# Kernel tuning notes

Measured on AMD Instinct MI355X. Metric: run time of the kernel, lower is better.

## Reference

```python
import jax, jax.numpy as jnp
import numpy as np
from jax import lax

B = 32768
D_IN = 512
D_DENSE = 256
T, F = 16, 16
H1, H2 = 128, 32
N_CLASSES = 10
BN_EPS = 1e-3


def _lstm_scan(xs, Wx, Wh, b):
    """Keras-style LSTM. xs: [B,T,F]; Wx: [F,4H]; Wh: [H,4H]; b: [4H].
    Gate order (Keras): i, f, g(candidate), o. Returns hs: [T,B,H]."""
    Bn = xs.shape[0]
    H = Wh.shape[0]
    # precompute input projections for all timesteps (one big GEMM)
    zx = jnp.einsum('btf,fg->tbg', xs, Wx) + b  # [T,B,4H]

    def step(carry, zx_t):
        h, c = carry
        z = zx_t + h @ Wh  # [B,4H]
        i, f, g, o = jnp.split(z, 4, axis=-1)
        i = jax.nn.sigmoid(i)
        f = jax.nn.sigmoid(f)
        g = jnp.tanh(g)
        o = jax.nn.sigmoid(o)
        c = f * c + i * g
        h = o * jnp.tanh(c)
        return (h, c), h

    h0 = jnp.zeros((Bn, H), xs.dtype)
    c0 = jnp.zeros((Bn, H), xs.dtype)
    (_, _), hs = lax.scan(step, (h0, c0), zx)
    return hs  # [T,B,H]


def setup_inputs() -> dict:
    key = jax.random.key(0)
    ks = jax.random.split(key, 12)
    s = lambda *sh: 1.0 / np.sqrt(sh[0])
    inp = {
        'x': jax.random.normal(ks[0], (B, D_IN), jnp.float32),
        'W_d1': jax.random.normal(ks[1], (D_IN, D_DENSE), jnp.float32) * s(D_IN),
        'b_d1': jnp.zeros((D_DENSE,), jnp.float32),
        'bn_gamma': jnp.ones((D_DENSE,), jnp.float32),
        'bn_beta': jnp.zeros((D_DENSE,), jnp.float32),
        'bn_mean': jax.random.normal(ks[2], (D_DENSE,), jnp.float32) * 0.1,
        'bn_var': jax.random.uniform(ks[3], (D_DENSE,), jnp.float32, 0.5, 1.5),
        'Wx1': jax.random.normal(ks[4], (F, 4 * H1), jnp.float32) * s(F),
        'Wh1': jax.random.normal(ks[5], (H1, 4 * H1), jnp.float32) * s(H1),
        'b1': jnp.zeros((4 * H1,), jnp.float32),
        'Wx2': jax.random.normal(ks[6], (H1, 4 * H2), jnp.float32) * s(H1),
        'Wh2': jax.random.normal(ks[7], (H2, 4 * H2), jnp.float32) * s(H2),
        'b2': jnp.zeros((4 * H2,), jnp.float32),
        'W_d2': jax.random.normal(ks[8], (H2, N_CLASSES), jnp.float32) * s(H2),
        'b_d2': jnp.zeros((N_CLASSES,), jnp.float32),
    }
    return inp


def reference(x, W_d1, b_d1, bn_gamma, bn_beta, bn_mean, bn_var,
              Wx1, Wh1, b1, Wx2, Wh2, b2, W_d2, b_d2):
    # Dense(256)
    h = x @ W_d1 + b_d1  # [B,256]
    # BatchNorm (inference: moving stats), eps=1e-3 (Keras default)
    h = (h - bn_mean) * (bn_gamma * lax.rsqrt(bn_var + BN_EPS)) + bn_beta
    # LeakyReLU(0.2)
    h = jnp.where(h >= 0, h, 0.2 * h)
    # Reshape to [B,16,16]
    seq = h.reshape(-1, T, F)
    # LSTM(128, return_sequences=True); dropout is inference no-op
    hs1 = _lstm_scan(seq, Wx1, Wh1, b1)            # [T,B,128]
    # LSTM(32, return_sequences=False)
    hs2 = _lstm_scan(jnp.swapaxes(hs1, 0, 1), Wx2, Wh2, b2)  # [T,B,32]
    h_last = hs2[-1]                                # [B,32]
    # Dense(10, softmax)
    logits = h_last @ W_d2 + b_d2
    return jax.nn.softmax(logits, axis=-1)
```

## Files before the change

### kernel.cpp

```cpp
#include <hip/hip_runtime.h>
#include <hip/hip_bf16.h>
#include <stdint.h>


typedef short bf16x8 __attribute__((ext_vector_type(8)));
typedef float f32x4 __attribute__((ext_vector_type(4)));
typedef unsigned short ushort_t;

#define NTHR 512

__device__ __forceinline__ ushort_t f2bf(float f) {
    unsigned u = __float_as_uint(f);
    u = u + 0x7fffu + ((u >> 16) & 1u);
    return (ushort_t)(u >> 16);
}
__device__ __forceinline__ float bf2f(ushort_t h) {
    return __uint_as_float(((unsigned)h) << 16);
}
__device__ __forceinline__ ushort_t planev(float v, int plane) {
    ushort_t hi = f2bf(v);
    if (plane == 0) return hi;
    return f2bf(v - bf2f(hi));
}
__device__ __forceinline__ int foff(int nt, int KC, int kc, int plane, int lane) {
    return (((nt * KC + kc) * 2 + plane) * 64 + lane) * 8;
}
__device__ __forceinline__ f32x4 mfma16(bf16x8 a, bf16x8 b, f32x4 c) {
    return __builtin_amdgcn_mfma_f32_16x16x32_bf16(a, b, c, 0, 0, 0);
}
__device__ __forceinline__ float sigm(float x) { return 1.0f / (1.0f + __expf(-x)); }
__device__ __forceinline__ float tanhc(float x) {
    x = fminf(15.0f, fmaxf(-15.0f, x));
    float e = __expf(2.0f * x);
    return (e - 1.0f) / (e + 1.0f);
}

__global__ void prep_weights(const float* __restrict__ Wd1, const float* __restrict__ Wx1,
                             const float* __restrict__ Wh1, const float* __restrict__ Wx2,
                             const float* __restrict__ Wh2, const float* __restrict__ Wd2,
                             ushort_t* __restrict__ wd1f, ushort_t* __restrict__ wh1f,
                             ushort_t* __restrict__ wx1f, ushort_t* __restrict__ w2f,
                             ushort_t* __restrict__ wd2f) {
    const int i = blockIdx.x * blockDim.x + threadIdx.x;
    const int j = i & 7;
    const int lane = (i >> 3) & 63;
    const int plane = (i >> 9) & 1;
    const int rest = i >> 10;
    const int krow = ((lane >> 4) << 3) + j;
    const int ncol = lane & 15;
    {
        const int kc = rest & 15, nt = rest >> 4;
        const int k = kc * 32 + krow, n = nt * 16 + ncol;
        wd1f[i] = planev(Wd1[k * 256 + n], plane);
    }
    if (i < 131072) {
        const int kc = rest & 3, nt = rest >> 2;
        const int k = kc * 32 + krow, n = nt * 16 + ncol;
        wh1f[i] = planev(Wh1[k * 512 + n], plane);
    }
    if (i < 32768) {
        const int nt = rest;
        const int k = krow, n = nt * 16 + ncol;
        const float v = (k < 16) ? Wx1[k * 512 + n] : 0.f;
        wx1f[i] = planev(v, plane);
    }
    if (i < 40960) {
        const int kc = rest % 5, nt = rest / 5;
        const int k = kc * 32 + krow, n = nt * 16 + ncol;
        const float v = (k < 32) ? Wh2[k * 128 + n] : Wx2[(k - 32) * 128 + n];
        w2f[i] = planev(v, plane);
    }
    if (i < 1024) {
        const int k = krow, n = ncol;
        const float v = (n < 10) ? Wd2[k * 10 + n] : 0.f;
        wd2f[i] = planev(v, plane);
    }
}

__global__ __launch_bounds__(NTHR, 2) void dense1_kernel(
    const float* __restrict__ X, const float* __restrict__ bd1,
    const float* __restrict__ gam, const float* __restrict__ bet,
    const float* __restrict__ mu, const float* __restrict__ var,
    const ushort_t* __restrict__ wd1f, ushort_t* __restrict__ sfrag) {
    __shared__ __align__(16) ushort_t Xs[2][64][40];
    const int tid = threadIdx.x;
    const int lane = tid & 63, w = tid >> 6;
    const int l4 = lane >> 4, l15 = lane & 15;
    const int blk = blockIdx.x;
    const long rowbase = (long)blk * 64;

    float bias[2];
#pragma unroll
    for (int ct = 0; ct < 2; ++ct) bias[ct] = bd1[w * 32 + ct * 16 + l15];
    f32x4 acc[4][2];
#pragma unroll
    for (int rt = 0; rt < 4; ++rt)
#pragma unroll
        for (int ct = 0; ct < 2; ++ct) { f32x4 a = {bias[ct], bias[ct], bias[ct], bias[ct]}; acc[rt][ct] = a; }

    const int srow = tid >> 3;
    const int sc4 = tid & 7;

#pragma unroll 1
    for (int kc = 0; kc < 16; ++kc) {
        if (kc) __syncthreads();
        const float4 xv = *reinterpret_cast<const float4*>(X + (rowbase + srow) * 512 + kc * 32 + sc4 * 4);
        float x4[4] = {xv.x, xv.y, xv.z, xv.w};
        ushort_t hs[4], ls[4];
#pragma unroll
        for (int q = 0; q < 4; ++q) { hs[q] = f2bf(x4[q]); ls[q] = f2bf(x4[q] - bf2f(hs[q])); }
        *reinterpret_cast<ushort4*>(&Xs[0][srow][sc4 * 4]) = make_ushort4(hs[0], hs[1], hs[2], hs[3]);
        *reinterpret_cast<ushort4*>(&Xs[1][srow][sc4 * 4]) = make_ushort4(ls[0], ls[1], ls[2], ls[3]);
        __syncthreads();

        bf16x8 Ah[4], Al[4];
#pragma unroll
        for (int rt = 0; rt < 4; ++rt) {
            Ah[rt] = *reinterpret_cast<const bf16x8*>(&Xs[0][rt * 16 + l15][l4 * 8]);
            Al[rt] = *reinterpret_cast<const bf16x8*>(&Xs[1][rt * 16 + l15][l4 * 8]);
        }
#pragma unroll
        for (int ct = 0; ct < 2; ++ct) {
            const int nt = w * 2 + ct;
            bf16x8 Bh = *reinterpret_cast<const bf16x8*>(wd1f + foff(nt, 16, kc, 0, lane));
            bf16x8 Bl = *reinterpret_cast<const bf16x8*>(wd1f + foff(nt, 16, kc, 1, lane));
#pragma unroll
            for (int rt = 0; rt < 4; ++rt) {
                acc[rt][ct] = mfma16(Ah[rt], Bh, acc[rt][ct]);
                acc[rt][ct] = mfma16(Ah[rt], Bl, acc[rt][ct]);
                acc[rt][ct] = mfma16(Al[rt], Bh, acc[rt][ct]);
            }
        }
    }

#pragma unroll
    for (int ct = 0; ct < 2; ++ct) {
        const int col = w * 32 + ct * 16 + l15;
        const float sc = gam[col] * rsqrtf(var[col] + 1e-3f);
        const float sh = bet[col] - mu[col] * sc;
        const int t = col >> 4, f = col & 15;
        const int jp = f & 7;
#pragma unroll
        for (int rt = 0; rt < 4; ++rt) {
            const long rtg = (long)blk * 4 + rt;
#pragma unroll
            for (int jd = 0; jd < 4; ++jd) {
                float v = acc[rt][ct][jd] * sc + sh;
                v = (v >= 0.f) ? v : 0.2f * v;
                const int rowin = l4 * 4 + jd;
                const int lanep = rowin + ((f >> 3) << 4);
                const long base = (((rtg * 16 + t) * 2 + 0) * 32 + lanep) * 8 + jp;
                const ushort_t hi = f2bf(v);
                sfrag[base] = hi;
                sfrag[base + 256] = f2bf(v - bf2f(hi));
            }
        }
    }
}

__global__ __launch_bounds__(NTHR, 1) void lstm_kernel(
    const ushort_t* __restrict__ wh1f, const ushort_t* __restrict__ wx1f,
    const ushort_t* __restrict__ w2f, const ushort_t* __restrict__ wd2f,
    const ushort_t* __restrict__ sfrag, const float* __restrict__ b1,
    const float* __restrict__ b2, const float* __restrict__ bd2,
    float* __restrict__ out) {
    __shared__ __align__(16) ushort_t A[2][64][168];
    __shared__ float C1[64][132];
    const int tid = threadIdx.x;
    const int lane = tid & 63, w = tid >> 6;
    const int l4 = lane >> 4, l15 = lane & 15;
    const int blk = blockIdx.x;

    {
        unsigned long long* p = (unsigned long long*)&A[0][0][0];
#pragma unroll 4
        for (int i = tid; i < 2 * 64 * 168 / 4; i += NTHR) p[i] = 0ull;
        float* q = &C1[0][0];
#pragma unroll 4
        for (int i = tid; i < 64 * 132; i += NTHR) q[i] = 0.f;
    }

    float c2[4];
#pragma unroll
    for (int q = 0; q < 4; ++q) c2[q] = 0.f;

    const int u1 = w * 16 + l15;
    float b1g[4];
#pragma unroll
    for (int g = 0; g < 4; ++g) b1g[g] = b1[g * 128 + u1];
    const int rt2 = w & 3;
    const int u2base = (w >> 2) * 16;
    float b2g[4];
#pragma unroll
    for (int g = 0; g < 4; ++g) b2g[g] = b2[g * 32 + u2base + l15];

    __syncthreads();

#pragma unroll 1
    for (int t = 0; t < 16; ++t) {
        f32x4 acc1[4][4];
#pragma unroll
        for (int rt = 0; rt < 4; ++rt)
#pragma unroll
            for (int g = 0; g < 4; ++g) { f32x4 a = {b1g[g], b1g[g], b1g[g], b1g[g]}; acc1[rt][g] = a; }

#pragma unroll
        for (int kc = 0; kc < 4; ++kc) {
            bf16x8 Ah[4], Al[4];
#pragma unroll
            for (int rt = 0; rt < 4; ++rt) {
                Ah[rt] = *reinterpret_cast<const bf16x8*>(&A[0][rt * 16 + l15][32 + kc * 32 + l4 * 8]);
                Al[rt] = *reinterpret_cast<const bf16x8*>(&A[1][rt * 16 + l15][32 + kc * 32 + l4 * 8]);
            }
#pragma unroll
            for (int g = 0; g < 4; ++g) {
                const int nt = g * 8 + w;
                bf16x8 Bh = *reinterpret_cast<const bf16x8*>(wh1f + foff(nt, 4, kc, 0, lane));
                bf16x8 Bl = *reinterpret_cast<const bf16x8*>(wh1f + foff(nt, 4, kc, 1, lane));
#pragma unroll
                for (int rt = 0; rt < 4; ++rt) {
                    acc1[rt][g] = mfma16(Ah[rt], Bh, acc1[rt][g]);
                    acc1[rt][g] = mfma16(Ah[rt], Bl, acc1[rt][g]);
                    acc1[rt][g] = mfma16(Al[rt], Bh, acc1[rt][g]);
                }
            }
        }
        {
            bf16x8 Sh[4], Sl[4];
#pragma unroll
            for (int rt = 0; rt < 4; ++rt) {
                bf16x8 z = {};
                Sh[rt] = z; Sl[rt] = z;
                if (lane < 32) {
                    const long rtg = (long)blk * 4 + rt;
                    const long so = (((rtg * 16 + t) * 2 + 0) * 32 + lane) * 8;
                    Sh[rt] = *reinterpret_cast<const bf16x8*>(sfrag + so);
                    Sl[rt] = *reinterpret_cast<const bf16x8*>(sfrag + so + 256);
                }
            }
#pragma unroll
            for (int g = 0; g < 4; ++g) {
                const int nt = g * 8 + w;
                bf16x8 Bh = *reinterpret_cast<const bf16x8*>(wx1f + foff(nt, 1, 0, 0, lane));
                bf16x8 Bl = *reinterpret_cast<const bf16x8*>(wx1f + foff(nt, 1, 0, 1, lane));
#pragma unroll
                for (int rt = 0; rt < 4; ++rt) {
                    acc1[rt][g] = mfma16(Sh[rt], Bh, acc1[rt][g]);
                    acc1[rt][g] = mfma16(Sh[rt], Bl, acc1[rt][g]);
                    acc1[rt][g] = mfma16(Sl[rt], Bh, acc1[rt][g]);
                }
            }
        }
        __syncthreads();
#pragma unroll
        for (int rt = 0; rt < 4; ++rt) {
#pragma unroll
            for (int jd = 0; jd < 4; ++jd) {
                const int row = rt * 16 + l4 * 4 + jd;
                const float ig = sigm(acc1[rt][0][jd]);
                const float fg = sigm(acc1[rt][1][jd]);
                const float gg = tanhc(acc1[rt][2][jd]);
                const float og = sigm(acc1[rt][3][jd]);
                const float c = fg * C1[row][u1] + ig * gg;
                C1[row][u1] = c;
                const float v = og * tanhc(c);
                const ushort_t hi = f2bf(v);
                A[0][row][32 + u1] = hi;
                A[1][row][32 + u1] = f2bf(v - bf2f(hi));
            }
        }
        __syncthreads();
        f32x4 acc2[4];
#pragma unroll
        for (int g = 0; g < 4; ++g) { f32x4 a = {b2g[g], b2g[g], b2g[g], b2g[g]}; acc2[g] = a; }
#pragma unroll
        for (int kc = 0; kc < 5; ++kc) {
            bf16x8 Ah2 = *reinterpret_cast<const bf16x8*>(&A[0][rt2 * 16 + l15][kc * 32 + l4 * 8]);
            bf16x8 Al2 = *reinterpret_cast<const bf16x8*>(&A[1][rt2 * 16 + l15][kc * 32 + l4 * 8]);
#pragma unroll
            for (int g = 0; g < 4; ++g) {
                const int nt = g * 2 + (w >> 2);
                bf16x8 Bh = *reinterpret_cast<const bf16x8*>(w2f + foff(nt, 5, kc, 0, lane));
                bf16x8 Bl = *reinterpret_cast<const bf16x8*>(w2f + foff(nt, 5, kc, 1, lane));
                acc2[g] = mfma16(Ah2, Bh, acc2[g]);
                acc2[g] = mfma16(Ah2, Bl, acc2[g]);
                acc2[g] = mfma16(Al2, Bh, acc2[g]);
            }
        }
        float hn2[4];
#pragma unroll
        for (int jd = 0; jd < 4; ++jd) {
            const float ig = sigm(acc2[0][jd]);
            const float fg = sigm(acc2[1][jd]);
            const float gg = tanhc(acc2[2][jd]);
            const float og = sigm(acc2[3][jd]);
            const float c = fg * c2[jd] + ig * gg;
            c2[jd] = c;
            hn2[jd] = og * tanhc(c);
        }
        __syncthreads();
#pragma unroll
        for (int jd = 0; jd < 4; ++jd) {
            const int row = rt2 * 16 + l4 * 4 + jd;
            const float v = hn2[jd];
            const ushort_t hi = f2bf(v);
            A[0][row][u2base + l15] = hi;
            A[1][row][u2base + l15] = f2bf(v - bf2f(hi));
        }
    }
    __syncthreads();

    if (w < 4) {
        const int rt = w;
        bf16x8 Ah2 = *reinterpret_cast<const bf16x8*>(&A[0][rt * 16 + l15][l4 * 8]);
        bf16x8 Al2 = *reinterpret_cast<const bf16x8*>(&A[1][rt * 16 + l15][l4 * 8]);
        bf16x8 Bh = *reinterpret_cast<const bf16x8*>(wd2f + foff(0, 1, 0, 0, lane));
        bf16x8 Bl = *reinterpret_cast<const bf16x8*>(wd2f + foff(0, 1, 0, 1, lane));
        const float bb = (l15 < 10) ? bd2[l15] : 0.f;
        f32x4 accd = {bb, bb, bb, bb};
        accd = mfma16(Ah2, Bh, accd);
        accd = mfma16(Ah2, Bl, accd);
        accd = mfma16(Al2, Bh, accd);
#pragma unroll
        for (int jd = 0; jd < 4; ++jd) {
            float v = (l15 < 10) ? accd[jd] : -1e30f;
            float m = v;
            m = fmaxf(m, __shfl_xor(m, 1));
            m = fmaxf(m, __shfl_xor(m, 2));
            m = fmaxf(m, __shfl_xor(m, 4));
            m = fmaxf(m, __shfl_xor(m, 8));
            float e = (l15 < 10) ? __expf(v - m) : 0.f;
            float s = e;
            s += __shfl_xor(s, 1);
            s += __shfl_xor(s, 2);
            s += __shfl_xor(s, 4);
            s += __shfl_xor(s, 8);
            if (l15 < 10) {
                const long r = (long)blk * 64 + rt * 16 + l4 * 4 + jd;
                out[r * 10 + l15] = e / s;
            }
        }
    }
}

extern "C" void kernel_launch(void* const* d_in, const int* in_sizes, int n_in,
                              void* d_out, int out_size, void* d_ws, size_t ws_size,
                              hipStream_t stream) {
    const float* x   = (const float*)d_in[0];
    const float* Wd1 = (const float*)d_in[1];
    const float* bd1 = (const float*)d_in[2];
    const float* gam = (const float*)d_in[3];
    const float* bet = (const float*)d_in[4];
    const float* mu  = (const float*)d_in[5];
    const float* var = (const float*)d_in[6];
    const float* Wx1 = (const float*)d_in[7];
    const float* Wh1 = (const float*)d_in[8];
    const float* b1  = (const float*)d_in[9];
    const float* Wx2 = (const float*)d_in[10];
    const float* Wh2 = (const float*)d_in[11];
    const float* b2  = (const float*)d_in[12];
    const float* Wd2 = (const float*)d_in[13];
    const float* bd2 = (const float*)d_in[14];
    float* out = (float*)d_out;

    char* ws = (char*)d_ws;
    ushort_t* wd1f  = (ushort_t*)(ws);
    ushort_t* wh1f  = (ushort_t*)(ws + 524288);
    ushort_t* wx1f  = (ushort_t*)(ws + 786432);
    ushort_t* w2f   = (ushort_t*)(ws + 851968);
    ushort_t* wd2f  = (ushort_t*)(ws + 933888);
    ushort_t* sfrag = (ushort_t*)(ws + 935936);

    hipLaunchKernelGGL(prep_weights, dim3(512), dim3(512), 0, stream,
                       Wd1, Wx1, Wh1, Wx2, Wh2, Wd2, wd1f, wh1f, wx1f, w2f, wd2f);
    hipLaunchKernelGGL(dense1_kernel, dim3(512), dim3(512), 0, stream,
                       x, bd1, gam, bet, mu, var, wd1f, sfrag);
    hipLaunchKernelGGL(lstm_kernel, dim3(512), dim3(512), 0, stream,
                       wh1f, wx1f, w2f, wd2f, sfrag, b1, b2, bd2, out);
}
```

Before: 971.9 us.

## Split LSTM1 gate GEMM into two row-tile passes with early activation

The layer-1 recurrent GEMM is split into two passes of two row tiles each. Each pass computes its gate activations and cell update right away and packs the hi/lo bf16 parts of h into registers. The writes to shared memory are delayed until after the barrier. This halves the live accumulator count, from 64 to 32 f32x4, to cut register pressure. It also lets the transcendental math of the first pass overlap with the MFMAs of the second, though the sched_barrier between passes limits how much interleaving the compiler can do.

```diff
diff --git a/kernel.cpp b/kernel.cpp
--- a/kernel.cpp
+++ b/kernel.cpp
@@ -158,6 +158,84 @@
     }
 }
 
+#define Z1_PASS(RT0)                                                                              \
+    {                                                                                             \
+        f32x4 acc[2][4];                                                                          \
+        _Pragma("unroll")                                                                         \
+        for (int r2 = 0; r2 < 2; ++r2)                                                            \
+            _Pragma("unroll")                                                                     \
+            for (int g = 0; g < 4; ++g) {                                                         \
+                f32x4 a = {b1g[g], b1g[g], b1g[g], b1g[g]};                                       \
+                acc[r2][g] = a;                                                                   \
+            }                                                                                     \
+        _Pragma("unroll")                                                                         \
+        for (int kc = 0; kc < 4; ++kc) {                                                          \
+            bf16x8 Ah[2], Al[2];                                                                  \
+            _Pragma("unroll")                                                                     \
+            for (int r2 = 0; r2 < 2; ++r2) {                                                      \
+                Ah[r2] = *reinterpret_cast<const bf16x8*>(                                        \
+                    &A[0][(RT0 + r2) * 16 + l15][32 + kc * 32 + l4 * 8]);                         \
+                Al[r2] = *reinterpret_cast<const bf16x8*>(                                        \
+                    &A[1][(RT0 + r2) * 16 + l15][32 + kc * 32 + l4 * 8]);                         \
+            }                                                                                     \
+            _Pragma("unroll")                                                                     \
+            for (int g = 0; g < 4; ++g) {                                                         \
+                const int nt = g * 8 + w;                                                         \
+                bf16x8 Bh = *reinterpret_cast<const bf16x8*>(wh1f + foff(nt, 4, kc, 0, lane));    \
+                bf16x8 Bl = *reinterpret_cast<const bf16x8*>(wh1f + foff(nt, 4, kc, 1, lane));    \
+                _Pragma("unroll")                                                                 \
+                for (int r2 = 0; r2 < 2; ++r2) {                                                  \
+                    acc[r2][g] = mfma16(Ah[r2], Bh, acc[r2][g]);                                  \
+                    acc[r2][g] = mfma16(Ah[r2], Bl, acc[r2][g]);                                  \
+                    acc[r2][g] = mfma16(Al[r2], Bh, acc[r2][g]);                                  \
+                }                                                                                 \
+            }                                                                                     \
+        }                                                                                         \
+        {                                                                                         \
+            bf16x8 Sh[2], Sl[2];                                                                  \
+            _Pragma("unroll")                                                                     \
+            for (int r2 = 0; r2 < 2; ++r2) {                                                      \
+                bf16x8 z = {};                                                                    \
+                Sh[r2] = z; Sl[r2] = z;                                                           \
+                if (lane < 32) {                                                                  \
+                    const long rtg = (long)blk * 4 + (RT0 + r2);                                  \
+                    const long so = (((rtg * 16 + t) * 2 + 0) * 32 + lane) * 8;                   \
+                    Sh[r2] = *reinterpret_cast<const bf16x8*>(sfrag + so);                        \
+                    Sl[r2] = *reinterpret_cast<const bf16x8*>(sfrag + so + 256);                  \
+                }                                                                                 \
+            }                                                                                     \
+            _Pragma("unroll")                                                                     \
+            for (int g = 0; g < 4; ++g) {                                                         \
+                const int nt = g * 8 + w;                                                         \
+                bf16x8 Bh = *reinterpret_cast<const bf16x8*>(wx1f + foff(nt, 1, 0, 0, lane));     \
+                bf16x8 Bl = *reinterpret_cast<const bf16x8*>(wx1f + foff(nt, 1, 0, 1, lane));     \
+                _Pragma("unroll")                                                                 \
+                for (int r2 = 0; r2 < 2; ++r2) {                                                  \
+                    acc[r2][g] = mfma16(Sh[r2], Bh, acc[r2][g]);                                  \
+                    acc[r2][g] = mfma16(Sh[r2], Bl, acc[r2][g]);                                  \
+                    acc[r2][g] = mfma16(Sl[r2], Bh, acc[r2][g]);                                  \
+                }                                                                                 \
+            }                                                                                     \
+        }                                                                                         \
+        _Pragma("unroll")                                                                         \
+        for (int r2 = 0; r2 < 2; ++r2) {                                                          \
+            _Pragma("unroll")                                                                     \
+            for (int jd = 0; jd < 4; ++jd) {                                                      \
+                const int row = (RT0 + r2) * 16 + l4 * 4 + jd;              \
+                const float ig = sigm(acc[r2][0][jd]);                                            \
+                const float fg = sigm(acc[r2][1][jd]);                                            \
+                const float gg = tanhc(acc[r2][2][jd]);                                           \
+                const float og = sigm(acc[r2][3][jd]);                                            \
+                const float c = fg * C1[row][u1] + ig * gg;                                       \
+                C1[row][u1] = c;                                                                  \
+                const float v = og * tanhc(c);                                                    \
+                const ushort_t hi = f2bf(v);                                                      \
+                const ushort_t lo = f2bf(v - bf2f(hi));                                           \
+                hpk[RT0 + r2][jd] = (unsigned)hi | ((unsigned)lo << 16);                          \
+            }                                                                                     \
+        }                                                                                         \
+    }
+
 __global__ __launch_bounds__(NTHR, 1) void lstm_kernel(
     const ushort_t* __restrict__ wh1f, const ushort_t* __restrict__ wx1f,
     const ushort_t* __restrict__ w2f, const ushort_t* __restrict__ wd2f,
@@ -198,75 +276,19 @@
 
 #pragma unroll 1
     for (int t = 0; t < 16; ++t) {
-        f32x4 acc1[4][4];
-#pragma unroll
-        for (int rt = 0; rt < 4; ++rt)
-#pragma unroll
-            for (int g = 0; g < 4; ++g) { f32x4 a = {b1g[g], b1g[g], b1g[g], b1g[g]}; acc1[rt][g] = a; }
-
-#pragma unroll
-        for (int kc = 0; kc < 4; ++kc) {
-            bf16x8 Ah[4], Al[4];
-#pragma unroll
-            for (int rt = 0; rt < 4; ++rt) {
-                Ah[rt] = *reinterpret_cast<const bf16x8*>(&A[0][rt * 16 + l15][32 + kc * 32 + l4 * 8]);
-                Al[rt] = *reinterpret_cast<const bf16x8*>(&A[1][rt * 16 + l15][32 + kc * 32 + l4 * 8]);
-            }
-#pragma unroll
-            for (int g = 0; g < 4; ++g) {
-                const int nt = g * 8 + w;
-                bf16x8 Bh = *reinterpret_cast<const bf16x8*>(wh1f + foff(nt, 4, kc, 0, lane));
-                bf16x8 Bl = *reinterpret_cast<const bf16x8*>(wh1f + foff(nt, 4, kc, 1, lane));
-#pragma unroll
-                for (int rt = 0; rt < 4; ++rt) {
-                    acc1[rt][g] = mfma16(Ah[rt], Bh, acc1[rt][g]);
-                    acc1[rt][g] = mfma16(Ah[rt], Bl, acc1[rt][g]);
-                    acc1[rt][g] = mfma16(Al[rt], Bh, acc1[rt][g]);
-                }
-            }
-        }
-        {
-            bf16x8 Sh[4], Sl[4];
-#pragma unroll
-            for (int rt = 0; rt < 4; ++rt) {
-                bf16x8 z = {};
-                Sh[rt] = z; Sl[rt] = z;
-                if (lane < 32) {
-                    const long rtg = (long)blk * 4 + rt;
-                    const long so = (((rtg * 16 + t) * 2 + 0) * 32 + lane) * 8;
-                    Sh[rt] = *reinterpret_cast<const bf16x8*>(sfrag + so);
-                    Sl[rt] = *reinterpret_cast<const bf16x8*>(sfrag + so + 256);
-                }
-            }
-#pragma unroll
-            for (int g = 0; g < 4; ++g) {
-                const int nt = g * 8 + w;
-                bf16x8 Bh = *reinterpret_cast<const bf16x8*>(wx1f + foff(nt, 1, 0, 0, lane));
-                bf16x8 Bl = *reinterpret_cast<const bf16x8*>(wx1f + foff(nt, 1, 0, 1, lane));
-#pragma unroll
-                for (int rt = 0; rt < 4; ++rt) {
-                    acc1[rt][g] = mfma16(Sh[rt], Bh, acc1[rt][g]);
-                    acc1[rt][g] = mfma16(Sh[rt], Bl, acc1[rt][g]);
-                    acc1[rt][g] = mfma16(Sl[rt], Bh, acc1[rt][g]);
-                }
-            }
-        }
+        unsigned hpk[4][4];
+        Z1_PASS(0)
+        __builtin_amdgcn_sched_barrier(0);
+        Z1_PASS(2)
         __syncthreads();
 #pragma unroll
         for (int rt = 0; rt < 4; ++rt) {
 #pragma unroll
             for (int jd = 0; jd < 4; ++jd) {
                 const int row = rt * 16 + l4 * 4 + jd;
-                const float ig = sigm(acc1[rt][0][jd]);
-                const float fg = sigm(acc1[rt][1][jd]);
-                const float gg = tanhc(acc1[rt][2][jd]);
-                const float og = sigm(acc1[rt][3][jd]);
-                const float c = fg * C1[row][u1] + ig * gg;
-                C1[row][u1] = c;
-                const float v = og * tanhc(c);
-                const ushort_t hi = f2bf(v);
-                A[0][row][32 + u1] = hi;
-                A[1][row][32 + u1] = f2bf(v - bf2f(hi));
+                const unsigned p = hpk[rt][jd];
+                A[0][row][32 + u1] = (ushort_t)(p & 0xffffu);
+                A[1][row][32 + u1] = (ushort_t)(p >> 16);
             }
         }
         __syncthreads();
```

Result: faster. 904.3 us (-7.0%).
